# Optimization experiments

Measured on AMD Instinct MI355X. Metric: run time of the kernel, lower is better.

Reference implementation:

```python
import jax, jax.numpy as jnp
import numpy as np

N = 50000      # nodes per type
E = 800000     # edges per relation
F_IN = 256
HID = 256
OUT = 128


def _edges(k):
    e = jax.random.randint(k, (2, E), 0, N)
    src, dst = e[0], e[1]
    # ensure no pre-existing self loops (PyG adds remaining self loops itself)
    src = jnp.where(src == dst, (src + 1) % N, src)
    return jnp.stack([src, dst]).astype(jnp.int64)


def _w(k, i, o):
    return (jax.random.normal(k, (i, o), jnp.float32) / np.float32(np.sqrt(i)))


def setup_inputs() -> dict:
    key = jax.random.key(0)
    ks = jax.random.split(key, 40)
    inp = {
        'x_lnc_jac': jax.random.normal(ks[0], (N, F_IN), jnp.float32),
        'x_prot_jac': jax.random.normal(ks[1], (N, F_IN), jnp.float32),
        'x_lnc_blast': jax.random.normal(ks[2], (N, F_IN), jnp.float32),
        'x_prot_blast': jax.random.normal(ks[3], (N, F_IN), jnp.float32),
        'edge_jac_lnc': _edges(ks[4]),
        'edge_jac_prot': _edges(ks[5]),
        'edge_blast_lnc': _edges(ks[6]),
        'edge_blast_prot': _edges(ks[7]),
        # jaccard view GCN weights (layer1: F_IN->HID, layer2: HID->OUT)
        'W_j1_lnc': _w(ks[8], F_IN, HID), 'b_j1_lnc': jnp.zeros((HID,), jnp.float32),
        'W_j1_prot': _w(ks[9], F_IN, HID), 'b_j1_prot': jnp.zeros((HID,), jnp.float32),
        'W_j2_lnc': _w(ks[10], HID, OUT), 'b_j2_lnc': jnp.zeros((OUT,), jnp.float32),
        'W_j2_prot': _w(ks[11], HID, OUT), 'b_j2_prot': jnp.zeros((OUT,), jnp.float32),
        # blast view GCN weights
        'W_b1_lnc': _w(ks[12], F_IN, HID), 'b_b1_lnc': jnp.zeros((HID,), jnp.float32),
        'W_b1_prot': _w(ks[13], F_IN, HID), 'b_b1_prot': jnp.zeros((HID,), jnp.float32),
        'W_b2_lnc': _w(ks[14], HID, OUT), 'b_b2_lnc': jnp.zeros((OUT,), jnp.float32),
        'W_b2_prot': _w(ks[15], HID, OUT), 'b_b2_prot': jnp.zeros((OUT,), jnp.float32),
        # residual linears
        'W_res_lnc': _w(ks[16], F_IN, OUT), 'b_res_lnc': jnp.zeros((OUT,), jnp.float32),
        'W_res_prot': _w(ks[17], F_IN, OUT), 'b_res_prot': jnp.zeros((OUT,), jnp.float32),
    }
    return inp


def _gcn(x, edge_index, W, b):
    # PyG GCNConv: add self loops, sym-normalize, transform, scatter-add, +bias
    src, dst = edge_index[0], edge_index[1]
    n = x.shape[0]
    xw = x @ W                                             # [N, F_out]
    ones = jnp.ones((src.shape[0],), xw.dtype)
    deg = jax.ops.segment_sum(ones, dst, num_segments=n) + 1.0  # in-deg + self loop
    dinv = jax.lax.rsqrt(deg)
    coef = (dinv[src] * dinv[dst])[:, None]
    agg = jax.ops.segment_sum(xw[src] * coef, dst, num_segments=n)
    return agg + xw / deg[:, None] + b                      # self-loop norm = 1/deg


def _lrelu(x):
    return jnp.where(x >= 0, x, 0.2 * x)


def reference(x_lnc_jac, x_prot_jac, x_lnc_blast, x_prot_blast,
              edge_jac_lnc, edge_jac_prot, edge_blast_lnc, edge_blast_prot,
              W_j1_lnc, b_j1_lnc, W_j1_prot, b_j1_prot,
              W_j2_lnc, b_j2_lnc, W_j2_prot, b_j2_prot,
              W_b1_lnc, b_b1_lnc, W_b1_prot, b_b1_prot,
              W_b2_lnc, b_b2_lnc, W_b2_prot, b_b2_prot,
              W_res_lnc, b_res_lnc, W_res_prot, b_res_prot):
    # jaccard view: 2 GCN layers per node type (HeteroConv mean over a single
    # relation per destination type is identity)
    h = _lrelu(_gcn(x_lnc_jac, edge_jac_lnc, W_j1_lnc, b_j1_lnc))
    jl = _lrelu(_gcn(h, edge_jac_lnc, W_j2_lnc, b_j2_lnc))
    h = _lrelu(_gcn(x_prot_jac, edge_jac_prot, W_j1_prot, b_j1_prot))
    jp = _lrelu(_gcn(h, edge_jac_prot, W_j2_prot, b_j2_prot))
    # blast view
    h = _lrelu(_gcn(x_lnc_blast, edge_blast_lnc, W_b1_lnc, b_b1_lnc))
    bl = _lrelu(_gcn(h, edge_blast_lnc, W_b2_lnc, b_b2_lnc))
    h = _lrelu(_gcn(x_prot_blast, edge_blast_prot, W_b1_prot, b_b1_prot))
    bp = _lrelu(_gcn(h, edge_blast_prot, W_b2_prot, b_b2_prot))
    # fuse views + residual from the ORIGINAL jaccard features
    comb_l = (jl + bl) * 0.5 + (x_lnc_jac @ W_res_lnc + b_res_lnc)
    comb_p = (jp + bp) * 0.5 + (x_prot_jac @ W_res_prot + b_res_prot)
    return (comb_l, comb_p, jl, jp, bl, bp)
```

## Files before the change

### kernel.cpp

```cpp
#include <hip/hip_runtime.h>
#include <cstddef>

#define NN 50000
#define NE 800000

typedef __bf16 bf16x8 __attribute__((ext_vector_type(8)));
typedef float floatx4 __attribute__((ext_vector_type(4)));

__device__ __forceinline__ float bflo2f(unsigned int u) {
    union { unsigned int u; float f; } v; v.u = u << 16; return v.f;
}
__device__ __forceinline__ float bfhi2f(unsigned int u) {
    union { unsigned int u; float f; } v; v.u = u & 0xffff0000u; return v.f;
}
__device__ __forceinline__ unsigned short f2bf(float f) {
    union { float f; unsigned int u; } v; v.f = f;
    unsigned int u = v.u;
    unsigned int r = u + 0x7fffu + ((u >> 16) & 1u);
    return (unsigned short)(r >> 16);
}


__global__ void k_count(const int* __restrict__ e0, const int* __restrict__ e1,
                        const int* __restrict__ e2, const int* __restrict__ e3,
                        int* __restrict__ counts) {
    const int* es[4] = {e0, e1, e2, e3};
    int r = blockIdx.y;
    int i = blockIdx.x * blockDim.x + threadIdx.x;
    if (i < NE) {
        int d = es[r][NE + i];
        atomicAdd(&counts[r * NN + d], 1);
    }
}

__global__ void k_deg(const int* __restrict__ counts, float* __restrict__ dinv, int total) {
    int i = blockIdx.x * blockDim.x + threadIdx.x;
    if (i < total) {
        float d = (float)(counts[i] + 1);
        dinv[i] = rsqrtf(d);
    }
}

#define SCH 256
__global__ void k_scan_a(const int* __restrict__ counts, int* __restrict__ bsum, int n) {
    __shared__ int sd[SCH];
    int r = blockIdx.y, b = blockIdx.x, t = threadIdx.x;
    int i = b * SCH + t;
    int v = (i < n) ? counts[r * n + i] : 0;
    sd[t] = v; __syncthreads();
    for (int o = 1; o < SCH; o <<= 1) {
        int x = (t >= o) ? sd[t - o] : 0; __syncthreads();
        sd[t] += x; __syncthreads();
    }
    if (t == SCH - 1) bsum[r * gridDim.x + b] = sd[t];
}
__global__ void k_scan_b(int* __restrict__ bsum, int nch) {
    __shared__ int sd[SCH];
    int r = blockIdx.y, t = threadIdx.x;
    int v = (t < nch) ? bsum[r * nch + t] : 0;
    sd[t] = v; __syncthreads();
    for (int o = 1; o < SCH; o <<= 1) {
        int x = (t >= o) ? sd[t - o] : 0; __syncthreads();
        sd[t] += x; __syncthreads();
    }
    if (t < nch) bsum[r * nch + t] = sd[t] - v;
}
__global__ void k_scan_c(const int* __restrict__ counts, const int* __restrict__ bsum,
                         int* __restrict__ rowptr, int n, int nch) {
    __shared__ int sd[SCH];
    int r = blockIdx.y, b = blockIdx.x, t = threadIdx.x;
    int i = b * SCH + t;
    int v = (i < n) ? counts[r * n + i] : 0;
    sd[t] = v; __syncthreads();
    for (int o = 1; o < SCH; o <<= 1) {
        int x = (t >= o) ? sd[t - o] : 0; __syncthreads();
        sd[t] += x; __syncthreads();
    }
    if (i < n) {
        int off = bsum[r * nch + b] + sd[t] - v;
        rowptr[r * (n + 1) + i] = off;
    }
    if (b == 0 && t == 0) rowptr[r * (n + 1) + n] = NE;
}


#define NBUK 98
#define BSH  9
#define ACH  4096
#define BCAP 12288

__global__ void k_binit(const int* __restrict__ rowptr, int* __restrict__ bfill) {
    int i = blockIdx.x * blockDim.x + threadIdx.x;
    if (i < 4 * 128) {
        int r = i >> 7, b = i & 127;
        int node = b << BSH; if (node > NN) node = NN;
        bfill[i] = rowptr[r * (NN + 1) + node];
    }
}

__global__ __launch_bounds__(256) void k_bucketA(
        const int* __restrict__ e0, const int* __restrict__ e1,
        const int* __restrict__ e2, const int* __restrict__ e3,
        int* __restrict__ bfill, uint2* __restrict__ pairbuf) {
    __shared__ int lcnt[128];
    __shared__ int s1[128];
    __shared__ int lbase[128];
    __shared__ int lfil[128];
    __shared__ int gbase[128];
    __shared__ uint2 sbuf[ACH];

    const int* es[4] = {e0, e1, e2, e3};
    const int r = blockIdx.y;
    const int tid = threadIdx.x;
    const int* src = es[r];
    const int* dst = es[r] + NE;
    const int lo = blockIdx.x * ACH;
    int hi = lo + ACH; if (hi > NE) hi = NE;
    const int cnt = hi - lo;

    if (tid < 128) lcnt[tid] = 0;
    __syncthreads();

    for (int i = lo + tid; i < hi; i += 256)
        atomicAdd(&lcnt[dst[i] >> BSH], 1);
    __syncthreads();

    if (tid < 128) s1[tid] = lcnt[tid];
    __syncthreads();
    for (int o = 1; o < 128; o <<= 1) {
        int x = (tid < 128 && tid >= o) ? s1[tid - o] : 0;
        __syncthreads();
        if (tid < 128) s1[tid] += x;
        __syncthreads();
    }
    if (tid < 128) {
        int eb = s1[tid] - lcnt[tid];
        lbase[tid] = eb;
        lfil[tid] = eb;
    }
    __syncthreads();

    for (int i = lo + tid; i < hi; i += 256) {
        int d = dst[i];
        int b = d >> BSH;
        int p = atomicAdd(&lfil[b], 1);
        uint2 v; v.x = (unsigned int)src[i]; v.y = (unsigned int)d;
        sbuf[p] = v;
    }
    __syncthreads();

    if (tid < 128 && lcnt[tid] > 0)
        gbase[tid] = atomicAdd(&bfill[r * 128 + tid], lcnt[tid]);
    __syncthreads();

    uint2* pout = pairbuf + (size_t)r * NE;
    for (int i = tid; i < cnt; i += 256) {
        int loB = 0, hiB = 128;
        while (hiB - loB > 1) {
            int m = (loB + hiB) >> 1;
            if (lbase[m] <= i) loB = m; else hiB = m;
        }
        pout[(size_t)gbase[loB] + (i - lbase[loB])] = sbuf[i];
    }
}

__global__ __launch_bounds__(256) void k_bucketB(
        const uint2* __restrict__ pairbuf, const int* __restrict__ rowptr,
        int* __restrict__ csr_src) {
    __shared__ int csrimg[BCAP];
    __shared__ int lfil[512];

    const int r = blockIdx.y;
    const int b = blockIdx.x;
    const int tid = threadIdx.x;
    const int node_lo = b << BSH;
    int node_hi = node_lo + 512; if (node_hi > NN) node_hi = NN;
    const int* rp = rowptr + r * (NN + 1);
    const int seg0 = rp[node_lo];
    const int seg1 = rp[node_hi];
    const int nr = node_hi - node_lo;

    for (int j = tid; j < nr; j += 256) lfil[j] = rp[node_lo + j] - seg0;
    __syncthreads();

    const uint2* pb = pairbuf + (size_t)r * NE;
    for (int i = seg0 + tid; i < seg1; i += 256) {
        uint2 p = pb[i];
        int li = (int)p.y - node_lo;
        if (li >= 0 && li < 512) {
            int s = atomicAdd(&lfil[li], 1);
            if (s >= 0 && s < BCAP) csrimg[s] = (int)p.x;
        }
    }
    __syncthreads();

    int* co = csr_src + (size_t)r * NE + seg0;
    const int n = seg1 - seg0;
    for (int k = tid; k < n; k += 256) co[k] = csrimg[k];
}


struct WTArgs {
    const float* W[10];
    unsigned short* Wt[10];
    int M[10];
};

__global__ void k_wT_all(WTArgs a) {
    int g = blockIdx.y;
    int M = a.M[g];
    int total = 256 * M;
    int i = blockIdx.x * blockDim.x + threadIdx.x;
    if (i < total) {
        int m = i >> 8, k = i & 255;
        a.Wt[g][i] = f2bf(a.W[g][(size_t)k * M + m]);
    }
}

#define GB_BM 128
#define GB_BN 128
#define GB_BK 32

template <bool AF32>
__global__ __launch_bounds__(256) void k_gemm(
        const void* __restrict__ Aptr, const unsigned short* __restrict__ Bt,
        int nrows, int K, int ncols,
        unsigned short* __restrict__ outBf, float* __restrict__ outF,
        const float* __restrict__ add0, const float* __restrict__ add1,
        const float* __restrict__ bias, int mode) {
    __shared__ __align__(16) unsigned short As[GB_BM][GB_BK];
    __shared__ __align__(16) unsigned short Bs[GB_BN][GB_BK];
    const int tid = threadIdx.x;
    const int lane = tid & 63;
    const int wid = tid >> 6;
    const int wm = (wid >> 1) * 64;
    const int wn = (wid & 1) * 64;
    const int row0 = blockIdx.x * GB_BM;
    const int col0 = blockIdx.y * GB_BN;
    const int lrow = lane & 15;
    const int lquad = lane >> 4;

    floatx4 acc[4][4];
#pragma unroll
    for (int i = 0; i < 4; i++)
#pragma unroll
        for (int j = 0; j < 4; j++) acc[i][j] = (floatx4){0.f, 0.f, 0.f, 0.f};

    for (int k0 = 0; k0 < K; k0 += GB_BK) {
#pragma unroll
        for (int t = 0; t < 2; t++) {
            int c = tid + t * 256;
            int r = c >> 2;
            int co = (c & 3) * 8;
            int gr = row0 + r; if (gr >= nrows) gr = nrows - 1;
            if constexpr (AF32) {
                const float* pa = (const float*)Aptr + (size_t)gr * K + k0 + co;
                float4 v0 = *(const float4*)pa;
                float4 v1 = *(const float4*)(pa + 4);
                uint4 o;
                o.x = (unsigned int)f2bf(v0.x) | ((unsigned int)f2bf(v0.y) << 16);
                o.y = (unsigned int)f2bf(v0.z) | ((unsigned int)f2bf(v0.w) << 16);
                o.z = (unsigned int)f2bf(v1.x) | ((unsigned int)f2bf(v1.y) << 16);
                o.w = (unsigned int)f2bf(v1.z) | ((unsigned int)f2bf(v1.w) << 16);
                *(uint4*)&As[r][co] = o;
            } else {
                *(uint4*)&As[r][co] =
                    *(const uint4*)((const unsigned short*)Aptr + (size_t)gr * K + k0 + co);
            }
            int gc = col0 + r;
            *(uint4*)&Bs[r][co] = *(const uint4*)(Bt + (size_t)gc * K + k0 + co);
        }
        __syncthreads();
        bf16x8 af[4], bfr[4];
#pragma unroll
        for (int i = 0; i < 4; i++) af[i] = *(const bf16x8*)&As[wm + 16 * i + lrow][lquad * 8];
#pragma unroll
        for (int j = 0; j < 4; j++) bfr[j] = *(const bf16x8*)&Bs[wn + 16 * j + lrow][lquad * 8];
#pragma unroll
        for (int i = 0; i < 4; i++)
#pragma unroll
            for (int j = 0; j < 4; j++)
                acc[i][j] = __builtin_amdgcn_mfma_f32_16x16x32_bf16(af[i], bfr[j], acc[i][j], 0, 0, 0);
        __syncthreads();
    }

#pragma unroll
    for (int i = 0; i < 4; i++) {
#pragma unroll
        for (int j = 0; j < 4; j++) {
            int col = col0 + wn + 16 * j + lrow;
#pragma unroll
            for (int r = 0; r < 4; r++) {
                int row = row0 + wm + 16 * i + lquad * 4 + r;
                if (row < nrows) {
                    float v = acc[i][j][r];
                    size_t idx = (size_t)row * ncols + col;
                    if (mode == 0) {
                        outBf[idx] = f2bf(v);
                    } else {
                        outF[idx] = v + bias[col] + 0.5f * (add0[idx] + add1[idx]);
                    }
                }
            }
        }
    }
}


__device__ __forceinline__ void ldrow4(const unsigned short* p, float* o) {
    uint2 r = *(const uint2*)p;
    o[0] = bflo2f(r.x & 0xffffu); o[1] = bfhi2f(r.x);
    o[2] = bflo2f(r.y & 0xffffu); o[3] = bfhi2f(r.y);
}
__device__ __forceinline__ void ldrow2(const unsigned short* p, float* o) {
    unsigned int r = *(const unsigned int*)p;
    o[0] = bflo2f(r & 0xffffu); o[1] = bfhi2f(r);
}

template <int NC>
__global__ __launch_bounds__(256) void k_aggregate(
        const unsigned short* __restrict__ xw,
        const int* __restrict__ rowptr,
        const int* __restrict__ cs,
        const float* __restrict__ dinv,
        const float* __restrict__ bias,
        unsigned short* __restrict__ outB,
        float* __restrict__ outF, int mode, int n) {
    constexpr int F = NC * 64;
    const int lane = threadIdx.x & 63;
    const int wid = blockIdx.x * (blockDim.x >> 6) + (threadIdx.x >> 6);
    const int nw = gridDim.x * (blockDim.x >> 6);
    const int fb = lane * NC;

    float bv[NC];
#pragma unroll
    for (int c = 0; c < NC; c++) bv[c] = bias[fb + c];

    for (int i = wid; i < n; i += nw) {
        float di = dinv[i];
        float acc[NC];
        {
            float rv[NC];
            if constexpr (NC == 4) ldrow4(xw + (size_t)i * F + fb, rv);
            else                   ldrow2(xw + (size_t)i * F + fb, rv);
#pragma unroll
            for (int c = 0; c < NC; c++) acc[c] = di * rv[c];
        }
        int e0 = rowptr[i], e1 = rowptr[i + 1];
        int j = e0;
        for (; j + 3 < e1; j += 4) {
            int s0 = cs[j], s1 = cs[j + 1], s2 = cs[j + 2], s3 = cs[j + 3];
            float c0 = dinv[s0], c1 = dinv[s1], c2 = dinv[s2], c3 = dinv[s3];
            float r0[NC], r1[NC], r2[NC], r3[NC];
            if constexpr (NC == 4) {
                ldrow4(xw + (size_t)s0 * F + fb, r0);
                ldrow4(xw + (size_t)s1 * F + fb, r1);
                ldrow4(xw + (size_t)s2 * F + fb, r2);
                ldrow4(xw + (size_t)s3 * F + fb, r3);
            } else {
                ldrow2(xw + (size_t)s0 * F + fb, r0);
                ldrow2(xw + (size_t)s1 * F + fb, r1);
                ldrow2(xw + (size_t)s2 * F + fb, r2);
                ldrow2(xw + (size_t)s3 * F + fb, r3);
            }
#pragma unroll
            for (int c = 0; c < NC; c++)
                acc[c] += c0 * r0[c] + c1 * r1[c] + c2 * r2[c] + c3 * r3[c];
        }
        for (; j < e1; j++) {
            int s = cs[j];
            float cf = dinv[s];
            float rv[NC];
            if constexpr (NC == 4) ldrow4(xw + (size_t)s * F + fb, rv);
            else                   ldrow2(xw + (size_t)s * F + fb, rv);
#pragma unroll
            for (int c = 0; c < NC; c++) acc[c] += cf * rv[c];
        }
#pragma unroll
        for (int c = 0; c < NC; c++) {
            float v = di * acc[c] + bv[c];
            acc[c] = v >= 0.f ? v : 0.2f * v;
        }
        if (mode == 0) {
            if constexpr (NC == 4) {
                uint2 o;
                o.x = (unsigned int)f2bf(acc[0]) | ((unsigned int)f2bf(acc[1]) << 16);
                o.y = (unsigned int)f2bf(acc[2]) | ((unsigned int)f2bf(acc[3]) << 16);
                *(uint2*)(outB + (size_t)i * F + fb) = o;
            } else {
                *(unsigned int*)(outB + (size_t)i * F + fb) =
                    (unsigned int)f2bf(acc[0]) | ((unsigned int)f2bf(acc[1]) << 16);
            }
        } else {
            if constexpr (NC == 4) {
                float4 o = {acc[0], acc[1], acc[2], acc[3]};
                *(float4*)(outF + (size_t)i * F + fb) = o;
            } else {
                float2 o = {acc[0], acc[1]};
                *(float2*)(outF + (size_t)i * F + fb) = o;
            }
        }
    }
}


static inline size_t alignup(size_t x) { return (x + 255) & ~(size_t)255; }

extern "C" void kernel_launch(void* const* d_in, const int* in_sizes, int n_in,
                              void* d_out, int out_size, void* d_ws, size_t ws_size,
                              hipStream_t stream) {
    const float* x[4]  = {(const float*)d_in[0], (const float*)d_in[1],
                          (const float*)d_in[2], (const float*)d_in[3]};
    const int* ed[4]   = {(const int*)d_in[4], (const int*)d_in[5],
                          (const int*)d_in[6], (const int*)d_in[7]};
    const float* W1[4] = {(const float*)d_in[8],  (const float*)d_in[10],
                          (const float*)d_in[16], (const float*)d_in[18]};
    const float* b1[4] = {(const float*)d_in[9],  (const float*)d_in[11],
                          (const float*)d_in[17], (const float*)d_in[19]};
    const float* W2[4] = {(const float*)d_in[12], (const float*)d_in[14],
                          (const float*)d_in[20], (const float*)d_in[22]};
    const float* b2[4] = {(const float*)d_in[13], (const float*)d_in[15],
                          (const float*)d_in[21], (const float*)d_in[23]};
    const float* Wr[2] = {(const float*)d_in[24], (const float*)d_in[26]};
    const float* br[2] = {(const float*)d_in[25], (const float*)d_in[27]};

    float* out = (float*)d_out;
    const size_t S = (size_t)NN * 128;

    char* w = (char*)d_ws;
    int*   counts  = (int*)w;                w += alignup((size_t)4 * NN * 4);
    int*   rowptr  = (int*)w;                w += alignup((size_t)4 * (NN + 1) * 4);
    float* dinv    = (float*)w;              w += alignup((size_t)4 * NN * 4);
    int*   bsum    = (int*)w;                w += alignup((size_t)4 * 256 * 4);
    int*   bfill   = (int*)w;                w += alignup((size_t)4 * 128 * 4);
    int*   csr_src = (int*)w;                w += alignup((size_t)4 * NE * 4);
    unsigned short* xw1 = (unsigned short*)w;  w += alignup((size_t)NN * 256 * 2);
    unsigned short* hbf = (unsigned short*)w;  w += alignup((size_t)NN * 256 * 2);
    unsigned short* xw2 = (unsigned short*)w;  w += alignup((size_t)NN * 128 * 2);
    unsigned short* WtA = (unsigned short*)w;  w += alignup((size_t)(4 * 256 * 256 + 6 * 128 * 256) * 2);

    uint2* pairbuf = (uint2*)xw1;

    unsigned short* Wt1[4], * Wt2[4], * Wtr[2];
    {
        unsigned short* p = WtA;
        for (int i = 0; i < 4; i++) { Wt1[i] = p; p += 256 * 256; }
        for (int i = 0; i < 4; i++) { Wt2[i] = p; p += 128 * 256; }
        for (int i = 0; i < 2; i++) { Wtr[i] = p; p += 128 * 256; }
    }

    hipMemsetAsync(counts, 0, (size_t)4 * NN * 4, stream);

    dim3 egrid((NE + 255) / 256, 4);
    k_count<<<egrid, 256, 0, stream>>>(ed[0], ed[1], ed[2], ed[3], counts);
    k_deg<<<(4 * NN + 255) / 256, 256, 0, stream>>>(counts, dinv, 4 * NN);
    int nch = (NN + SCH - 1) / SCH;
    k_scan_a<<<dim3(nch, 4), SCH, 0, stream>>>(counts, bsum, NN);
    k_scan_b<<<dim3(1, 4), SCH, 0, stream>>>(bsum, nch);
    k_scan_c<<<dim3(nch, 4), SCH, 0, stream>>>(counts, bsum, rowptr, NN, nch);

    k_binit<<<2, 256, 0, stream>>>(rowptr, bfill);
    k_bucketA<<<dim3((NE + ACH - 1) / ACH, 4), 256, 0, stream>>>(
            ed[0], ed[1], ed[2], ed[3], bfill, pairbuf);
    k_bucketB<<<dim3(NBUK, 4), 256, 0, stream>>>(pairbuf, rowptr, csr_src);

    {
        WTArgs a;
        for (int i = 0; i < 4; i++) { a.W[i] = W1[i];     a.Wt[i] = Wt1[i];     a.M[i] = 256; }
        for (int i = 0; i < 4; i++) { a.W[4 + i] = W2[i]; a.Wt[4 + i] = Wt2[i]; a.M[4 + i] = 128; }
        for (int i = 0; i < 2; i++) { a.W[8 + i] = Wr[i]; a.Wt[8 + i] = Wtr[i]; a.M[8 + i] = 128; }
        k_wT_all<<<dim3(256, 10), 256, 0, stream>>>(a);
    }

    const int gx = (NN + GB_BM - 1) / GB_BM;
    for (int p = 0; p < 4; p++) {
        const int* rp = rowptr + p * (NN + 1);
        const int* cs = csr_src + (size_t)p * NE;
        const float* dv = dinv + (size_t)p * NN;

        k_gemm<true><<<dim3(gx, 2), 256, 0, stream>>>(x[p], Wt1[p], NN, 256, 256,
                xw1, nullptr, nullptr, nullptr, nullptr, 0);
        k_aggregate<4><<<2048, 256, 0, stream>>>(xw1, rp, cs, dv, b1[p],
                hbf, nullptr, 0, NN);
        k_gemm<false><<<dim3(gx, 1), 256, 0, stream>>>(hbf, Wt2[p], NN, 256, 128,
                xw2, nullptr, nullptr, nullptr, nullptr, 0);
        k_aggregate<2><<<2048, 256, 0, stream>>>(xw2, rp, cs, dv, b2[p],
                nullptr, out + (2 + p) * S, 1, NN);
    }

    for (int t = 0; t < 2; t++) {
        const float* a0 = out + (2 + t) * S;
        const float* a1 = out + (4 + t) * S;
        k_gemm<true><<<dim3(gx, 1), 256, 0, stream>>>(x[t], Wtr[t], NN, 256, 128,
                nullptr, out + t * S, a0, a1, br[t], 1);
    }
}
```

Measured before the change: 1.175 ms.

## Build CSR from fixed-capacity buckets, dropping global count and scan passes

Removes the global degree count (atomics over all edges), the three-pass prefix scan and the memset. Bucket A now writes into fixed-capacity per-bucket slots, a tiny scan over bucket counts gives segment bases, and bucket B computes per-node counts, rowptr and dinv locally in shared memory. This drops several kernel launches and a full read of the edge arrays, but it relies on each 512-node bucket holding at most 12288 edges and truncates silently if one overflows.

```diff
diff --git a/kernel.cpp b/kernel.cpp
--- a/kernel.cpp
+++ b/kernel.cpp
@@ -21,81 +21,14 @@
 }
 
 
-__global__ void k_count(const int* __restrict__ e0, const int* __restrict__ e1,
-                        const int* __restrict__ e2, const int* __restrict__ e3,
-                        int* __restrict__ counts) {
-    const int* es[4] = {e0, e1, e2, e3};
-    int r = blockIdx.y;
-    int i = blockIdx.x * blockDim.x + threadIdx.x;
-    if (i < NE) {
-        int d = es[r][NE + i];
-        atomicAdd(&counts[r * NN + d], 1);
-    }
-}
-
-__global__ void k_deg(const int* __restrict__ counts, float* __restrict__ dinv, int total) {
-    int i = blockIdx.x * blockDim.x + threadIdx.x;
-    if (i < total) {
-        float d = (float)(counts[i] + 1);
-        dinv[i] = rsqrtf(d);
-    }
-}
-
-#define SCH 256
-__global__ void k_scan_a(const int* __restrict__ counts, int* __restrict__ bsum, int n) {
-    __shared__ int sd[SCH];
-    int r = blockIdx.y, b = blockIdx.x, t = threadIdx.x;
-    int i = b * SCH + t;
-    int v = (i < n) ? counts[r * n + i] : 0;
-    sd[t] = v; __syncthreads();
-    for (int o = 1; o < SCH; o <<= 1) {
-        int x = (t >= o) ? sd[t - o] : 0; __syncthreads();
-        sd[t] += x; __syncthreads();
-    }
-    if (t == SCH - 1) bsum[r * gridDim.x + b] = sd[t];
-}
-__global__ void k_scan_b(int* __restrict__ bsum, int nch) {
-    __shared__ int sd[SCH];
-    int r = blockIdx.y, t = threadIdx.x;
-    int v = (t < nch) ? bsum[r * nch + t] : 0;
-    sd[t] = v; __syncthreads();
-    for (int o = 1; o < SCH; o <<= 1) {
-        int x = (t >= o) ? sd[t - o] : 0; __syncthreads();
-        sd[t] += x; __syncthreads();
-    }
-    if (t < nch) bsum[r * nch + t] = sd[t] - v;
-}
-__global__ void k_scan_c(const int* __restrict__ counts, const int* __restrict__ bsum,
-                         int* __restrict__ rowptr, int n, int nch) {
-    __shared__ int sd[SCH];
-    int r = blockIdx.y, b = blockIdx.x, t = threadIdx.x;
-    int i = b * SCH + t;
-    int v = (i < n) ? counts[r * n + i] : 0;
-    sd[t] = v; __syncthreads();
-    for (int o = 1; o < SCH; o <<= 1) {
-        int x = (t >= o) ? sd[t - o] : 0; __syncthreads();
-        sd[t] += x; __syncthreads();
-    }
-    if (i < n) {
-        int off = bsum[r * nch + b] + sd[t] - v;
-        rowptr[r * (n + 1) + i] = off;
-    }
-    if (b == 0 && t == 0) rowptr[r * (n + 1) + n] = NE;
-}
-
-
 #define NBUK 98
 #define BSH  9
 #define ACH  4096
-#define BCAP 12288
-
-__global__ void k_binit(const int* __restrict__ rowptr, int* __restrict__ bfill) {
+#define BKCAP 12288
+
+__global__ void k_binit2(int* __restrict__ bfill) {
     int i = blockIdx.x * blockDim.x + threadIdx.x;
-    if (i < 4 * 128) {
-        int r = i >> 7, b = i & 127;
-        int node = b << BSH; if (node > NN) node = NN;
-        bfill[i] = rowptr[r * (NN + 1) + node];
-    }
+    if (i < 4 * 128) bfill[i] = (i & 127) * BKCAP;
 }
 
 __global__ __launch_bounds__(256) void k_bucketA(
@@ -153,7 +86,7 @@
         gbase[tid] = atomicAdd(&bfill[r * 128 + tid], lcnt[tid]);
     __syncthreads();
 
-    uint2* pout = pairbuf + (size_t)r * NE;
+    uint2* pout = pairbuf + (size_t)r * (128 * (size_t)BKCAP);
     for (int i = tid; i < cnt; i += 256) {
         int loB = 0, hiB = 128;
         while (hiB - loB > 1) {
@@ -164,39 +97,85 @@
     }
 }
 
+__global__ void k_bscan(const int* __restrict__ bfill, int* __restrict__ bbase,
+                        int* __restrict__ rowptr) {
+    __shared__ int sd[128];
+    int t = threadIdx.x;
+    for (int r = 0; r < 4; r++) {
+        int c = bfill[r * 128 + t] - t * BKCAP;
+        sd[t] = c; __syncthreads();
+        for (int o = 1; o < 128; o <<= 1) {
+            int x = (t >= o) ? sd[t - o] : 0; __syncthreads();
+            sd[t] += x; __syncthreads();
+        }
+        bbase[r * 128 + t] = sd[t] - c;
+        __syncthreads();
+    }
+    if (t == 0)
+        for (int r = 0; r < 4; r++) rowptr[r * (NN + 1) + NN] = NE;
+}
+
 __global__ __launch_bounds__(256) void k_bucketB(
-        const uint2* __restrict__ pairbuf, const int* __restrict__ rowptr,
-        int* __restrict__ csr_src) {
-    __shared__ int csrimg[BCAP];
-    __shared__ int lfil[512];
+        const uint2* __restrict__ pairbuf, const int* __restrict__ bfill,
+        const int* __restrict__ bbase, int* __restrict__ rowptr,
+        float* __restrict__ dinv, int* __restrict__ csr_src) {
+    __shared__ int csrimg[BKCAP];
+    __shared__ int lcnt[512];
+    __shared__ int lcur[512];
 
     const int r = blockIdx.y;
     const int b = blockIdx.x;
     const int tid = threadIdx.x;
     const int node_lo = b << BSH;
     int node_hi = node_lo + 512; if (node_hi > NN) node_hi = NN;
-    const int* rp = rowptr + r * (NN + 1);
-    const int seg0 = rp[node_lo];
-    const int seg1 = rp[node_hi];
     const int nr = node_hi - node_lo;
 
-    for (int j = tid; j < nr; j += 256) lfil[j] = rp[node_lo + j] - seg0;
-    __syncthreads();
-
-    const uint2* pb = pairbuf + (size_t)r * NE;
-    for (int i = seg0 + tid; i < seg1; i += 256) {
+    const int pbase = b * BKCAP;
+    int cnt = bfill[r * 128 + b] - pbase;
+    if (cnt > BKCAP) cnt = BKCAP;
+    const int seg0 = bbase[r * 128 + b];
+
+    lcnt[tid] = 0; lcnt[tid + 256] = 0;
+    __syncthreads();
+
+    const uint2* pb = pairbuf + (size_t)r * (128 * (size_t)BKCAP) + pbase;
+    for (int i = tid; i < cnt; i += 256) {
+        int li = (int)pb[i].y - node_lo;
+        if (li >= 0 && li < 512) atomicAdd(&lcnt[li], 1);
+    }
+    __syncthreads();
+    lcur[tid] = lcnt[tid]; lcur[tid + 256] = lcnt[tid + 256];
+    __syncthreads();
+    for (int o = 1; o < 512; o <<= 1) {
+        int a0 = (tid >= o) ? lcnt[tid - o] : 0;
+        int a1 = (tid + 256 >= o) ? lcnt[tid + 256 - o] : 0;
+        __syncthreads();
+        lcnt[tid] += a0; lcnt[tid + 256] += a1;
+        __syncthreads();
+    }
+#pragma unroll
+    for (int jj = 0; jj < 2; jj++) {
+        int j = tid + jj * 256;
+        int c = lcur[j];
+        int excl = lcnt[j] - c;
+        if (j < nr) {
+            rowptr[r * (NN + 1) + node_lo + j] = seg0 + excl;
+            dinv[r * NN + node_lo + j] = rsqrtf((float)(c + 1));
+        }
+        lcur[j] = excl;
+    }
+    __syncthreads();
+    for (int i = tid; i < cnt; i += 256) {
         uint2 p = pb[i];
         int li = (int)p.y - node_lo;
         if (li >= 0 && li < 512) {
-            int s = atomicAdd(&lfil[li], 1);
-            if (s >= 0 && s < BCAP) csrimg[s] = (int)p.x;
-        }
-    }
-    __syncthreads();
-
+            int s = atomicAdd(&lcur[li], 1);
+            if (s >= 0 && s < BKCAP) csrimg[s] = (int)p.x;
+        }
+    }
+    __syncthreads();
     int* co = csr_src + (size_t)r * NE + seg0;
-    const int n = seg1 - seg0;
-    for (int k = tid; k < n; k += 256) co[k] = csrimg[k];
+    for (int k = tid; k < cnt; k += 256) co[k] = csrimg[k];
 }
 
 
@@ -428,11 +407,10 @@
     const size_t S = (size_t)NN * 128;
 
     char* w = (char*)d_ws;
-    int*   counts  = (int*)w;                w += alignup((size_t)4 * NN * 4);
     int*   rowptr  = (int*)w;                w += alignup((size_t)4 * (NN + 1) * 4);
     float* dinv    = (float*)w;              w += alignup((size_t)4 * NN * 4);
-    int*   bsum    = (int*)w;                w += alignup((size_t)4 * 256 * 4);
     int*   bfill   = (int*)w;                w += alignup((size_t)4 * 128 * 4);
+    int*   bbase   = (int*)w;                w += alignup((size_t)4 * 128 * 4);
     int*   csr_src = (int*)w;                w += alignup((size_t)4 * NE * 4);
     unsigned short* xw1 = (unsigned short*)w;  w += alignup((size_t)NN * 256 * 2);
     unsigned short* hbf = (unsigned short*)w;  w += alignup((size_t)NN * 256 * 2);
@@ -449,20 +427,12 @@
         for (int i = 0; i < 2; i++) { Wtr[i] = p; p += 128 * 256; }
     }
 
-    hipMemsetAsync(counts, 0, (size_t)4 * NN * 4, stream);
-
-    dim3 egrid((NE + 255) / 256, 4);
-    k_count<<<egrid, 256, 0, stream>>>(ed[0], ed[1], ed[2], ed[3], counts);
-    k_deg<<<(4 * NN + 255) / 256, 256, 0, stream>>>(counts, dinv, 4 * NN);
-    int nch = (NN + SCH - 1) / SCH;
-    k_scan_a<<<dim3(nch, 4), SCH, 0, stream>>>(counts, bsum, NN);
-    k_scan_b<<<dim3(1, 4), SCH, 0, stream>>>(bsum, nch);
-    k_scan_c<<<dim3(nch, 4), SCH, 0, stream>>>(counts, bsum, rowptr, NN, nch);
-
-    k_binit<<<2, 256, 0, stream>>>(rowptr, bfill);
+    k_binit2<<<2, 256, 0, stream>>>(bfill);
     k_bucketA<<<dim3((NE + ACH - 1) / ACH, 4), 256, 0, stream>>>(
             ed[0], ed[1], ed[2], ed[3], bfill, pairbuf);
-    k_bucketB<<<dim3(NBUK, 4), 256, 0, stream>>>(pairbuf, rowptr, csr_src);
+    k_bscan<<<1, 128, 0, stream>>>(bfill, bbase, rowptr);
+    k_bucketB<<<dim3(NBUK, 4), 256, 0, stream>>>(pairbuf, bfill, bbase,
+            rowptr, dinv, csr_src);
 
     {
         WTArgs a;
```

Measured after the change: 1.057 ms. 1.11x faster.
